# Optimization experiments

Measured on AMD Instinct MI355X. Metric: run time of the kernel, lower is better.

## Reference

```python
import jax, jax.numpy as jnp
import numpy as np

N_NODES = 50000
N_EDGES = 800000
IN_DIM = 128
HIDDEN = 32
NHEAD = 4
OUT_DIM = 64
NEG_SLOPE = 0.2


def setup_inputs() -> dict:
    key = jax.random.key(0)
    ks = jax.random.split(key, 8)
    x = jax.random.normal(ks[0], (N_NODES, IN_DIM), dtype=jnp.float32)
    edge_index = jax.random.randint(ks[1], (2, N_EDGES), 0, N_NODES, dtype=jnp.int64)
    # layer 1: fc (in_dim -> nhead*hidden), attn [nhead, 2*hidden]
    W1 = jax.random.normal(ks[2], (IN_DIM, NHEAD * HIDDEN), dtype=jnp.float32) * 0.1
    attn1 = jax.random.normal(ks[3], (NHEAD, 2 * HIDDEN), dtype=jnp.float32) * 0.1
    # layer 2: fc (nhead*hidden -> 1*out_dim), attn [1, 2*out_dim]
    W2 = jax.random.normal(ks[4], (NHEAD * HIDDEN, OUT_DIM), dtype=jnp.float32) * 0.1
    attn2 = jax.random.normal(ks[5], (1, 2 * OUT_DIM), dtype=jnp.float32) * 0.1
    # extra output head: Linear(out_dim, out_dim) with bias
    head_W = jax.random.normal(ks[6], (OUT_DIM, OUT_DIM), dtype=jnp.float32) * 0.1
    head_b = jax.random.normal(ks[7], (OUT_DIM,), dtype=jnp.float32) * 0.1
    return {"x": x, "edge_index": edge_index, "W1": W1, "attn1": attn1,
            "W2": W2, "attn2": attn2, "head_W": head_W, "head_b": head_b}


def _gat_layer(x, W, attn, row, col, num_nodes, heads):
    """One GATConv: linear proj, edge attention, segment softmax over dst (col), scatter-add."""
    f_out = W.shape[1] // heads
    h = (x @ W).reshape(num_nodes, heads, f_out)            # [N, H, F]
    a_l, a_r = attn[:, :f_out], attn[:, f_out:]              # split attn for src/dst parts
    e_src = jnp.einsum('nhf,hf->nh', h, a_l)                 # [N, H]
    e_dst = jnp.einsum('nhf,hf->nh', h, a_r)                 # [N, H]
    alpha = e_src[row] + e_dst[col]                          # [E, H] == cat(h[row],h[col])·attn
    alpha = jax.nn.leaky_relu(alpha, NEG_SLOPE)
    # segment softmax grouped by destination node (col); self-loops guarantee non-empty segs
    amax = jax.ops.segment_max(alpha, col, num_segments=num_nodes)
    ex = jnp.exp(alpha - amax[col])
    denom = jax.ops.segment_sum(ex, col, num_segments=num_nodes)
    a = ex / denom[col]                                      # [E, H]
    msg = h[row] * a[:, :, None]                             # [E, H, F]
    out = jax.ops.segment_sum(msg, col, num_segments=num_nodes)  # [N, H, F]
    return out.reshape(num_nodes, heads * f_out)


def reference(x, edge_index, W1, attn1, W2, attn2, head_W, head_b):
    n = x.shape[0]
    loops = jnp.arange(n, dtype=edge_index.dtype)
    row = jnp.concatenate([edge_index[0], loops])
    col = jnp.concatenate([edge_index[1], loops])
    h = _gat_layer(x, W1, attn1, row, col, n, NHEAD)         # [N, NHEAD*HIDDEN]
    h = jax.nn.relu(h)                                       # intermediate-layer activation
    h = _gat_layer(h, W2, attn2, row, col, n, 1)             # [N, OUT_DIM] (last: no act)
    out = h @ head_W + head_b                                # extra_output_fc head
    return out
```

## Files before the change

kernel.cpp:

```cpp
#include <hip/hip_runtime.h>
#include <math.h>

#define N_NODES 50000
#define E_RAW 800000
#define E_TOT 850000
#define NEG_SLOPE 0.2f
#define G1_BLOCKS ((N_NODES + 63) / 64)
#define NBUCK 391
#define EPB 2048
#define PBLK ((E_TOT + EPB - 1) / EPB)

typedef __attribute__((ext_vector_type(8))) short bf16x8;
typedef __attribute__((ext_vector_type(4))) float f32x4;

__device__ __forceinline__ float lrelu(float a) { return a > 0.f ? a : NEG_SLOPE * a; }

__device__ __forceinline__ unsigned f2bf(float f) {
    unsigned u = __float_as_uint(f);
    return (u + 0x7fff + ((u >> 16) & 1)) >> 16;
}
__device__ __forceinline__ unsigned pack2(float a, float b) {
    return f2bf(a) | (f2bf(b) << 16);
}
__device__ __forceinline__ float bflo(unsigned p) { return __uint_as_float(p << 16); }
__device__ __forceinline__ float bfhi(unsigned p) { return __uint_as_float(p & 0xffff0000u); }

__global__ void k_prep(const float* __restrict__ W1, unsigned* __restrict__ Btg) {
    int c = blockIdx.x;
    int tq = threadIdx.x;
    Btg[c * 64 + tq] = pack2(W1[(2 * tq) * 128 + c], W1[(2 * tq + 1) * 128 + c]);
}

__global__ void k_prep2(const float* __restrict__ W2, const float* __restrict__ attn2,
                        const float* __restrict__ headW,
                        unsigned* __restrict__ Wctg, float* __restrict__ av) {
    int b = blockIdx.x, t = threadIdx.x;
    if (b < 64) {
        if (t < 64) {
            int f = b, q = t;
            float s0 = 0.f, s1 = 0.f;
            for (int j = 0; j < 64; ++j) {
                float hw = headW[j * 64 + f];
                s0 = fmaf(W2[(2 * q) * 64 + j], hw, s0);
                s1 = fmaf(W2[(2 * q + 1) * 64 + j], hw, s1);
            }
            Wctg[f * 64 + q] = pack2(s0, s1);
        }
    } else {
        int k = t;
        float sl = 0.f, sr = 0.f;
        for (int j = 0; j < 64; ++j) {
            float w = W2[k * 64 + j];
            sl = fmaf(w, attn2[j], sl);
            sr = fmaf(w, attn2[64 + j], sr);
        }
        av[k] = sl; av[128 + k] = sr;
    }
}

__global__ void k_gemm1_p1(const float* __restrict__ A, const unsigned* __restrict__ Btg,
                           const float* __restrict__ aux, uint2* __restrict__ C,
                           float* __restrict__ es, float* __restrict__ ed,
                           const int* __restrict__ ei, int* __restrict__ hist2d) {
    __shared__ unsigned As[64 * 64];
    if (blockIdx.x >= G1_BLOCKS) {
        int blk = blockIdx.x - G1_BLOCKS;
        int* h = (int*)As;
        for (int i = threadIdx.x; i < NBUCK; i += 256) h[i] = 0;
        __syncthreads();
        int base = blk * EPB;
        for (int i = threadIdx.x; i < EPB; i += 256) {
            int e = base + i;
            if (e >= E_TOT) break;
            int col = (e < E_RAW) ? ei[E_RAW + e] : (e - E_RAW);
            atomicAdd(&h[col >> 7], 1);
        }
        __syncthreads();
        for (int i = threadIdx.x; i < NBUCK; i += 256) hist2d[i * PBLK + blk] = h[i];
        return;
    }
    int t = threadIdx.x;
    int m0 = blockIdx.x * 64;
    int rows = min(64, N_NODES - m0);
    const float4* A4 = (const float4*)(A + (size_t)m0 * 128);
    for (int i = t; i < rows * 32; i += 256) {
        int row = i >> 5, k4 = i & 31;
        float4 v = A4[i];
        int byte = (k4 * 8) ^ ((row & 7) << 4);
        unsigned* p = &As[row * 64 + (byte >> 2)];
        p[0] = pack2(v.x, v.y);
        p[1] = pack2(v.z, v.w);
    }
    __syncthreads();
    int lane = t & 63, wave = t >> 6;
    int r15 = lane & 15, g = lane >> 4;
    int arow = wave * 16 + r15;
    f32x4 acc[8];
#pragma unroll
    for (int i = 0; i < 8; ++i) acc[i] = (f32x4){0.f, 0.f, 0.f, 0.f};
    const char* Abase = (const char*)As + arow * 256;
    int swz = (arow & 7) << 4;
    const char* Bbase = (const char*)Btg;
#pragma unroll
    for (int s = 0; s < 4; ++s) {
        bf16x8 xf = *(const bf16x8*)(Abase + ((64 * s + 16 * g) ^ swz));
#pragma unroll
        for (int tt = 0; tt < 8; ++tt) {
            bf16x8 wf = *(const bf16x8*)(Bbase + ((16 * tt + r15) * 256 + 64 * s + 16 * g));
            acc[tt] = __builtin_amdgcn_mfma_f32_16x16x32_bf16(wf, xf, acc[tt], 0, 0, 0);
        }
    }
    int grow = m0 + arow;
    bool valid = (arow < rows);
    if (valid) {
        uint2* C2 = C + (size_t)grow * 32;
#pragma unroll
        for (int tt = 0; tt < 8; ++tt) {
            uint2 v; v.x = pack2(acc[tt][0], acc[tt][1]); v.y = pack2(acc[tt][2], acc[tt][3]);
            C2[4 * tt + g] = v;
        }
    }
    float ps0 = 0.f, ps1 = 0.f, ps2 = 0.f, ps3 = 0.f;
    float pd0 = 0.f, pd1 = 0.f, pd2 = 0.f, pd3 = 0.f;
#pragma unroll
    for (int tt = 0; tt < 8; ++tt) {
        int h = tt >> 1;
        int fin = 16 * (tt & 1) + 4 * g;
        float4 alv = *(const float4*)(aux + h * 64 + fin);
        float4 arv = *(const float4*)(aux + h * 64 + 32 + fin);
        float s4 = acc[tt][0] * alv.x + acc[tt][1] * alv.y + acc[tt][2] * alv.z + acc[tt][3] * alv.w;
        float d4 = acc[tt][0] * arv.x + acc[tt][1] * arv.y + acc[tt][2] * arv.z + acc[tt][3] * arv.w;
        if (h == 0) { ps0 += s4; pd0 += d4; }
        else if (h == 1) { ps1 += s4; pd1 += d4; }
        else if (h == 2) { ps2 += s4; pd2 += d4; }
        else { ps3 += s4; pd3 += d4; }
    }
#pragma unroll
    for (int mask = 16; mask <= 32; mask <<= 1) {
        ps0 += __shfl_xor(ps0, mask); ps1 += __shfl_xor(ps1, mask);
        ps2 += __shfl_xor(ps2, mask); ps3 += __shfl_xor(ps3, mask);
        pd0 += __shfl_xor(pd0, mask); pd1 += __shfl_xor(pd1, mask);
        pd2 += __shfl_xor(pd2, mask); pd3 += __shfl_xor(pd3, mask);
    }
    if (valid) {
        float psg = (g == 0) ? ps0 : (g == 1) ? ps1 : (g == 2) ? ps2 : ps3;
        float pdg = (g == 0) ? pd0 : (g == 1) ? pd1 : (g == 2) ? pd2 : pd3;
        es[grow * 4 + g] = psg;
        ed[grow * 4 + g] = pdg;
    }
}

__global__ void k_p2a(const int* __restrict__ hist2d, int* __restrict__ off2d,
                      int* __restrict__ bucktot) {
    __shared__ int sh[512];
    int b = blockIdx.x, t = threadIdx.x;
    int v = (t < PBLK) ? hist2d[b * PBLK + t] : 0;
    sh[t] = v;
    __syncthreads();
    for (int ofs = 1; ofs < 512; ofs <<= 1) {
        int u = (t >= ofs) ? sh[t - ofs] : 0;
        __syncthreads();
        sh[t] += u;
        __syncthreads();
    }
    if (t < PBLK) off2d[b * PBLK + t] = sh[t] - v;
    if (t == 511) bucktot[b] = sh[511];
}

__global__ void k_p3(const int* __restrict__ ei, const int* __restrict__ off2d,
                     const int* __restrict__ bucktot, unsigned* __restrict__ part) {
    __shared__ int sh[512];
    __shared__ int h[NBUCK];
    __shared__ int basebuf[NBUCK];
    int blk = blockIdx.x, t = threadIdx.x;
    int v = (t < NBUCK) ? bucktot[t] : 0;
    sh[t] = v;
    if (t < NBUCK) h[t] = 0;
    __syncthreads();
    for (int ofs = 1; ofs < 512; ofs <<= 1) {
        int u = (t >= ofs) ? sh[t - ofs] : 0;
        __syncthreads();
        sh[t] += u;
        __syncthreads();
    }
    if (t < NBUCK) basebuf[t] = (sh[t] - v) + off2d[t * PBLK + blk];
    __syncthreads();
    int base = blk * EPB;
    for (int i = t; i < EPB; i += 512) {
        int e = base + i;
        if (e >= E_TOT) break;
        int col, src;
        if (e < E_RAW) { col = ei[E_RAW + e]; src = ei[e]; }
        else { col = src = e - E_RAW; }
        int b = col >> 7;
        int lr = atomicAdd(&h[b], 1);
        part[basebuf[b] + lr] = (unsigned)src | ((unsigned)(col & 127) << 16);
    }
}

__global__ void k_p4(const unsigned* __restrict__ part, const int* __restrict__ bucktot,
                     int* __restrict__ off, unsigned short* __restrict__ srcs) {
    __shared__ int sh[512];
    __shared__ int h[128];
    __shared__ int colofs[128];
    __shared__ int s0sh, s1sh;
    int b = blockIdx.x, t = threadIdx.x;
    int v = (t < NBUCK) ? bucktot[t] : 0;
    sh[t] = v;
    if (t < 128) h[t] = 0;
    __syncthreads();
    for (int ofs = 1; ofs < 512; ofs <<= 1) {
        int u = (t >= ofs) ? sh[t - ofs] : 0;
        __syncthreads();
        sh[t] += u;
        __syncthreads();
    }
    if (t == 0) { s1sh = sh[b]; s0sh = sh[b] - bucktot[b]; }
    __syncthreads();
    int s0 = s0sh, s1 = s1sh;
    for (int i = s0 + t; i < s1; i += 512) atomicAdd(&h[part[i] >> 16], 1);
    __syncthreads();
    if (t == 0) {
        int acc = 0;
        for (int c = 0; c < 128; ++c) { colofs[c] = acc; acc += h[c]; }
    }
    __syncthreads();
    int colbase = b * 128, ncols = min(128, N_NODES - colbase);
    if (t < ncols) off[colbase + t] = s0 + colofs[t];
    if (b == NBUCK - 1 && t == 0) off[N_NODES] = s1;
    if (t < 128) h[t] = colofs[t];
    __syncthreads();
    for (int i = s0 + t; i < s1; i += 512) {
        unsigned u = part[i];
        int c = u >> 16;
        int slot = atomicAdd(&h[c], 1);
        srcs[s0 + slot] = (unsigned short)(u & 0xffffu);
    }
}

__global__ void k_gemmv(const unsigned* __restrict__ A, const unsigned* __restrict__ Wctg,
                        uint2* __restrict__ C) {
    __shared__ unsigned As[64 * 64];
    int t = threadIdx.x;
    int m0 = blockIdx.x * 64;
    int rows = min(64, N_NODES - m0);
    const uint4* A4 = (const uint4*)(A + (size_t)m0 * 64);
    for (int i = t; i < rows * 16; i += 256) {
        int row = i >> 4, q = i & 15;
        uint4 v = A4[i];
        int byte = (q * 16) ^ ((row & 7) << 4);
        unsigned* p = &As[row * 64 + (byte >> 2)];
        p[0] = v.x; p[1] = v.y; p[2] = v.z; p[3] = v.w;
    }
    __syncthreads();
    int lane = t & 63, wave = t >> 6;
    int r15 = lane & 15, g = lane >> 4;
    int arow = wave * 16 + r15;
    f32x4 acc[4];
#pragma unroll
    for (int i = 0; i < 4; ++i) acc[i] = (f32x4){0.f, 0.f, 0.f, 0.f};
    const char* Abase = (const char*)As + arow * 256;
    int swz = (arow & 7) << 4;
    const char* Bbase = (const char*)Wctg;
#pragma unroll
    for (int s = 0; s < 4; ++s) {
        bf16x8 xf = *(const bf16x8*)(Abase + ((64 * s + 16 * g) ^ swz));
#pragma unroll
        for (int tt = 0; tt < 4; ++tt) {
            bf16x8 wf = *(const bf16x8*)(Bbase + ((16 * tt + r15) * 256 + 64 * s + 16 * g));
            acc[tt] = __builtin_amdgcn_mfma_f32_16x16x32_bf16(wf, xf, acc[tt], 0, 0, 0);
        }
    }
    int grow = m0 + arow;
    if (arow < rows) {
        uint2* C2 = C + (size_t)grow * 16;
#pragma unroll
        for (int tt = 0; tt < 4; ++tt) {
            uint2 v; v.x = pack2(acc[tt][0], acc[tt][1]); v.y = pack2(acc[tt][2], acc[tt][3]);
            C2[4 * tt + g] = v;
        }
    }
}

__global__ void k_agg1(const unsigned* __restrict__ h1b, const float* __restrict__ es,
                       const float* __restrict__ ed, const int* __restrict__ off,
                       const unsigned short* __restrict__ srcs, const float* __restrict__ av,
                       unsigned* __restrict__ out1,
                       float* __restrict__ e2s, float* __restrict__ e2d) {
    int n = blockIdx.x * (blockDim.x >> 6) + (threadIdx.x >> 6);
    int lane = threadIdx.x & 63;
    if (n >= N_NODES) return;
    int myh = lane & 3;
    int jj = lane >> 2;
    float edh = ed[n * 4 + myh];
    int s = off[n], e = off[n + 1];
    int l16 = lane & 15;
    int esub = lane >> 4;
    int hcL = l16 >> 2;
    float acc[8];
#pragma unroll
    for (int i = 0; i < 8; ++i) acc[i] = 0.f;
    float psum = 0.f;
    for (int base = s; base < e; base += 16) {
        int cnt = e - base;
        int srcj = 0;
        float w = 0.f;
        if (jj < cnt) {
            srcj = srcs[base + jj];
            w = __expf(lrelu(es[srcj * 4 + myh] + edh));
        }
        psum += w;
        int src4[4];
        float wv4[4];
#pragma unroll
        for (int q = 0; q < 4; ++q) {
            int eidx = 4 * q + esub;
            src4[q] = __shfl(srcj, eidx * 4);
            wv4[q] = __shfl(w, eidx * 4 + hcL);
        }
        uint4 pv4[4];
#pragma unroll
        for (int q = 0; q < 4; ++q)
            pv4[q] = *((const uint4*)(h1b + (size_t)src4[q] * 64 + l16 * 4));
#pragma unroll
        for (int q = 0; q < 4; ++q) {
            float wv = wv4[q];
            acc[0] = fmaf(bflo(pv4[q].x), wv, acc[0]);
            acc[1] = fmaf(bfhi(pv4[q].x), wv, acc[1]);
            acc[2] = fmaf(bflo(pv4[q].y), wv, acc[2]);
            acc[3] = fmaf(bfhi(pv4[q].y), wv, acc[3]);
            acc[4] = fmaf(bflo(pv4[q].z), wv, acc[4]);
            acc[5] = fmaf(bfhi(pv4[q].z), wv, acc[5]);
            acc[6] = fmaf(bflo(pv4[q].w), wv, acc[6]);
            acc[7] = fmaf(bfhi(pv4[q].w), wv, acc[7]);
        }
    }
#pragma unroll
    for (int mask = 4; mask <= 32; mask <<= 1) psum += __shfl_xor(psum, mask);
    float inv = 1.f / __shfl(psum, hcL);
#pragma unroll
    for (int i = 0; i < 8; ++i) {
        acc[i] += __shfl_xor(acc[i], 16);
        acc[i] += __shfl_xor(acc[i], 32);
    }
    float o[8];
#pragma unroll
    for (int i = 0; i < 8; ++i) o[i] = fmaxf(acc[i] * inv, 0.f);
    if (esub == 0) {
        uint4 ov;
        ov.x = pack2(o[0], o[1]);
        ov.y = pack2(o[2], o[3]);
        ov.z = pack2(o[4], o[5]);
        ov.w = pack2(o[6], o[7]);
        *((uint4*)(out1 + (size_t)n * 64 + l16 * 4)) = ov;
    }
    float4 vl0 = *(const float4*)(av + 8 * l16);
    float4 vl1 = *(const float4*)(av + 8 * l16 + 4);
    float4 vr0 = *(const float4*)(av + 128 + 8 * l16);
    float4 vr1 = *(const float4*)(av + 128 + 8 * l16 + 4);
    float pl = o[0] * vl0.x + o[1] * vl0.y + o[2] * vl0.z + o[3] * vl0.w
             + o[4] * vl1.x + o[5] * vl1.y + o[6] * vl1.z + o[7] * vl1.w;
    float pr = o[0] * vr0.x + o[1] * vr0.y + o[2] * vr0.z + o[3] * vr0.w
             + o[4] * vr1.x + o[5] * vr1.y + o[6] * vr1.z + o[7] * vr1.w;
#pragma unroll
    for (int mask = 1; mask <= 8; mask <<= 1) {
        pl += __shfl_xor(pl, mask);
        pr += __shfl_xor(pr, mask);
    }
    if (lane == 0) { e2s[n] = pl; e2d[n] = pr; }
}

__global__ void k_agg2f(const unsigned* __restrict__ v2b, const float* __restrict__ es,
                        const float* __restrict__ ed, const int* __restrict__ off,
                        const unsigned short* __restrict__ srcs,
                        const float* __restrict__ headb, float* __restrict__ outv) {
    int n = blockIdx.x * 4 + (threadIdx.x >> 6);
    int lane = threadIdx.x & 63;
    float edv = ed[n];
    int s = off[n], e = off[n + 1];
    int l16 = lane & 15;
    int esub = lane >> 4;
    const uint2* gp = (const uint2*)v2b;
    float a0 = 0.f, a1 = 0.f, a2 = 0.f, a3 = 0.f, psum = 0.f;
    for (int base = s; base < e; base += 16) {
        int cnt = e - base;
        int srcj = 0;
        float w = 0.f;
        if (lane < 16 && lane < cnt) {
            srcj = srcs[base + lane];
            w = __expf(lrelu(es[srcj] + edv));
        }
        psum += w;
        int src4[4];
        float wv4[4];
#pragma unroll
        for (int q = 0; q < 4; ++q) {
            int eidx = 4 * q + esub;
            src4[q] = __shfl(srcj, eidx);
            wv4[q] = __shfl(w, eidx);
        }
        uint2 pv4[4];
#pragma unroll
        for (int q = 0; q < 4; ++q) pv4[q] = gp[(size_t)src4[q] * 16 + l16];
#pragma unroll
        for (int q = 0; q < 4; ++q) {
            a0 = fmaf(bflo(pv4[q].x), wv4[q], a0);
            a1 = fmaf(bfhi(pv4[q].x), wv4[q], a1);
            a2 = fmaf(bflo(pv4[q].y), wv4[q], a2);
            a3 = fmaf(bfhi(pv4[q].y), wv4[q], a3);
        }
    }
#pragma unroll
    for (int mask = 1; mask <= 8; mask <<= 1) psum += __shfl_xor(psum, mask);
    float inv = 1.f / __shfl(psum, 0);
    a0 += __shfl_xor(a0, 16); a0 += __shfl_xor(a0, 32);
    a1 += __shfl_xor(a1, 16); a1 += __shfl_xor(a1, 32);
    a2 += __shfl_xor(a2, 16); a2 += __shfl_xor(a2, 32);
    a3 += __shfl_xor(a3, 16); a3 += __shfl_xor(a3, 32);
    if (esub == 0) {
        float4 bv = ((const float4*)headb)[l16];
        float4 o;
        o.x = fmaf(a0, inv, bv.x);
        o.y = fmaf(a1, inv, bv.y);
        o.z = fmaf(a2, inv, bv.z);
        o.w = fmaf(a3, inv, bv.w);
        ((float4*)outv)[(size_t)n * 16 + l16] = o;
    }
}

extern "C" void kernel_launch(void* const* d_in, const int* in_sizes, int n_in,
                              void* d_out, int out_size, void* d_ws, size_t ws_size,
                              hipStream_t stream) {
    const float* x     = (const float*)d_in[0];
    const int*   ei    = (const int*)d_in[1];
    const float* W1    = (const float*)d_in[2];
    const float* attn1 = (const float*)d_in[3];
    const float* W2    = (const float*)d_in[4];
    const float* attn2 = (const float*)d_in[5];
    const float* headW = (const float*)d_in[6];
    const float* headb = (const float*)d_in[7];
    float* out = (float*)d_out;

    char* ws = (char*)d_ws;
    size_t o = 0;
    auto alloc = [&](size_t bytes) -> void* {
        o = (o + 255) & ~(size_t)255;
        void* p = ws + o;
        o += bytes;
        return p;
    };
    unsigned*       h1b    = (unsigned*)alloc((size_t)N_NODES * 128 * 2);
    unsigned*       out1b  = (unsigned*)alloc((size_t)N_NODES * 128 * 2);
    unsigned*       v2b    = (unsigned*)alloc((size_t)N_NODES * 64 * 2);
    float*          e1s    = (float*)alloc((size_t)N_NODES * 4 * 4);
    float*          e1d    = (float*)alloc((size_t)N_NODES * 4 * 4);
    float*          e2s    = (float*)alloc((size_t)N_NODES * 4);
    float*          e2d    = (float*)alloc((size_t)N_NODES * 4);
    int*            off    = (int*)alloc((size_t)(N_NODES + 1) * 4);
    unsigned short* srcs   = (unsigned short*)alloc((size_t)E_TOT * 2);
    unsigned*       Btg    = (unsigned*)alloc((size_t)128 * 64 * 4);
    unsigned*       Wctg   = (unsigned*)alloc((size_t)64 * 64 * 4);
    float*          av     = (float*)alloc((size_t)256 * 4);
    int*            hist2d = (int*)alloc((size_t)NBUCK * PBLK * 4);
    int*            off2d  = (int*)alloc((size_t)NBUCK * PBLK * 4);
    int*            bucktot = (int*)alloc((size_t)NBUCK * 4);
    unsigned*       part   = (unsigned*)alloc((size_t)E_TOT * 4);

    k_prep<<<128, 64, 0, stream>>>(W1, Btg);
    k_prep2<<<65, 128, 0, stream>>>(W2, attn2, headW, Wctg, av);

    k_gemm1_p1<<<G1_BLOCKS + PBLK, 256, 0, stream>>>(
        x, Btg, attn1, (uint2*)h1b, e1s, e1d, ei, hist2d);

    k_p2a<<<NBUCK, 512, 0, stream>>>(hist2d, off2d, bucktot);
    k_p3<<<PBLK, 512, 0, stream>>>(ei, off2d, bucktot, part);
    k_p4<<<NBUCK, 512, 0, stream>>>(part, bucktot, off, srcs);

    k_agg1<<<N_NODES / 4, 256, 0, stream>>>(h1b, e1s, e1d, off, srcs, av, out1b, e2s, e2d);

    k_gemmv<<<(N_NODES + 63) / 64, 256, 0, stream>>>(out1b, Wctg, (uint2*)v2b);

    k_agg2f<<<N_NODES / 4, 256, 0, stream>>>(v2b, e2s, e2d, off, srcs, headb, out);
}
```

Before: 209.4 us.

## Fuse CSR build passes into one cooperative kernel and merge prep kernels

Merges the three CSR-construction kernels (bucket scan, partition, per-column sort) into a single cooperative kernel that uses grid-wide syncs in place of kernel boundaries. The two weight-prep kernels become one launch. In both aggregation kernels the neighbour feature gathers are now issued before the attention-weight exp computation, so memory latency overlaps the math. This saves launch overhead at the cost of grid.sync barriers, and requires all PBLK blocks of 512 threads to be co-resident.

```diff
diff --git a/kernel.cpp b/kernel.cpp
--- a/kernel.cpp
+++ b/kernel.cpp
@@ -1,5 +1,8 @@
 #include <hip/hip_runtime.h>
+#include <hip/hip_cooperative_groups.h>
 #include <math.h>
+
+namespace cg = cooperative_groups;
 
 #define N_NODES 50000
 #define E_RAW 800000
@@ -25,19 +28,16 @@
 __device__ __forceinline__ float bflo(unsigned p) { return __uint_as_float(p << 16); }
 __device__ __forceinline__ float bfhi(unsigned p) { return __uint_as_float(p & 0xffff0000u); }
 
-__global__ void k_prep(const float* __restrict__ W1, unsigned* __restrict__ Btg) {
-    int c = blockIdx.x;
-    int tq = threadIdx.x;
-    Btg[c * 64 + tq] = pack2(W1[(2 * tq) * 128 + c], W1[(2 * tq + 1) * 128 + c]);
-}
-
-__global__ void k_prep2(const float* __restrict__ W2, const float* __restrict__ attn2,
-                        const float* __restrict__ headW,
-                        unsigned* __restrict__ Wctg, float* __restrict__ av) {
+__global__ void k_prep(const float* __restrict__ W1, const float* __restrict__ W2,
+                       const float* __restrict__ attn2, const float* __restrict__ headW,
+                       unsigned* __restrict__ Btg, unsigned* __restrict__ Wctg,
+                       float* __restrict__ av) {
     int b = blockIdx.x, t = threadIdx.x;
-    if (b < 64) {
+    if (b < 128) {
+        if (t < 64) Btg[b * 64 + t] = pack2(W1[(2 * t) * 128 + b], W1[(2 * t + 1) * 128 + b]);
+    } else if (b < 192) {
         if (t < 64) {
-            int f = b, q = t;
+            int f = b - 128, q = t;
             float s0 = 0.f, s1 = 0.f;
             for (int j = 0; j < 64; ++j) {
                 float hw = headW[j * 64 + f];
@@ -150,91 +150,88 @@
     }
 }
 
-__global__ void k_p2a(const int* __restrict__ hist2d, int* __restrict__ off2d,
-                      int* __restrict__ bucktot) {
+__global__ void k_csr(const int* __restrict__ ei, const int* __restrict__ hist2d,
+                      int* __restrict__ off2d, int* __restrict__ bucktot,
+                      unsigned* __restrict__ part, int* __restrict__ off,
+                      unsigned short* __restrict__ srcs) {
+    cg::grid_group grid = cg::this_grid();
     __shared__ int sh[512];
-    int b = blockIdx.x, t = threadIdx.x;
-    int v = (t < PBLK) ? hist2d[b * PBLK + t] : 0;
-    sh[t] = v;
-    __syncthreads();
-    for (int ofs = 1; ofs < 512; ofs <<= 1) {
-        int u = (t >= ofs) ? sh[t - ofs] : 0;
-        __syncthreads();
-        sh[t] += u;
-        __syncthreads();
-    }
-    if (t < PBLK) off2d[b * PBLK + t] = sh[t] - v;
-    if (t == 511) bucktot[b] = sh[511];
-}
-
-__global__ void k_p3(const int* __restrict__ ei, const int* __restrict__ off2d,
-                     const int* __restrict__ bucktot, unsigned* __restrict__ part) {
-    __shared__ int sh[512];
-    __shared__ int h[NBUCK];
-    __shared__ int basebuf[NBUCK];
-    int blk = blockIdx.x, t = threadIdx.x;
-    int v = (t < NBUCK) ? bucktot[t] : 0;
-    sh[t] = v;
-    if (t < NBUCK) h[t] = 0;
-    __syncthreads();
-    for (int ofs = 1; ofs < 512; ofs <<= 1) {
-        int u = (t >= ofs) ? sh[t - ofs] : 0;
-        __syncthreads();
-        sh[t] += u;
-        __syncthreads();
-    }
-    if (t < NBUCK) basebuf[t] = (sh[t] - v) + off2d[t * PBLK + blk];
-    __syncthreads();
-    int base = blk * EPB;
-    for (int i = t; i < EPB; i += 512) {
-        int e = base + i;
-        if (e >= E_TOT) break;
-        int col, src;
-        if (e < E_RAW) { col = ei[E_RAW + e]; src = ei[e]; }
-        else { col = src = e - E_RAW; }
-        int b = col >> 7;
-        int lr = atomicAdd(&h[b], 1);
-        part[basebuf[b] + lr] = (unsigned)src | ((unsigned)(col & 127) << 16);
-    }
-}
-
-__global__ void k_p4(const unsigned* __restrict__ part, const int* __restrict__ bucktot,
-                     int* __restrict__ off, unsigned short* __restrict__ srcs) {
-    __shared__ int sh[512];
-    __shared__ int h[128];
-    __shared__ int colofs[128];
+    __shared__ int hh[NBUCK];
+    __shared__ int bb[NBUCK];
     __shared__ int s0sh, s1sh;
     int b = blockIdx.x, t = threadIdx.x;
-    int v = (t < NBUCK) ? bucktot[t] : 0;
-    sh[t] = v;
-    if (t < 128) h[t] = 0;
-    __syncthreads();
-    for (int ofs = 1; ofs < 512; ofs <<= 1) {
-        int u = (t >= ofs) ? sh[t - ofs] : 0;
-        __syncthreads();
-        sh[t] += u;
-        __syncthreads();
-    }
-    if (t == 0) { s1sh = sh[b]; s0sh = sh[b] - bucktot[b]; }
-    __syncthreads();
-    int s0 = s0sh, s1 = s1sh;
-    for (int i = s0 + t; i < s1; i += 512) atomicAdd(&h[part[i] >> 16], 1);
-    __syncthreads();
-    if (t == 0) {
-        int acc = 0;
-        for (int c = 0; c < 128; ++c) { colofs[c] = acc; acc += h[c]; }
-    }
-    __syncthreads();
-    int colbase = b * 128, ncols = min(128, N_NODES - colbase);
-    if (t < ncols) off[colbase + t] = s0 + colofs[t];
-    if (b == NBUCK - 1 && t == 0) off[N_NODES] = s1;
-    if (t < 128) h[t] = colofs[t];
-    __syncthreads();
-    for (int i = s0 + t; i < s1; i += 512) {
-        unsigned u = part[i];
-        int c = u >> 16;
-        int slot = atomicAdd(&h[c], 1);
-        srcs[s0 + slot] = (unsigned short)(u & 0xffffu);
+    if (b < NBUCK) {
+        int v = (t < PBLK) ? hist2d[b * PBLK + t] : 0;
+        sh[t] = v;
+        __syncthreads();
+        for (int ofs = 1; ofs < 512; ofs <<= 1) {
+            int u = (t >= ofs) ? sh[t - ofs] : 0;
+            __syncthreads();
+            sh[t] += u;
+            __syncthreads();
+        }
+        if (t < PBLK) off2d[b * PBLK + t] = sh[t] - v;
+        if (t == 511) bucktot[b] = sh[511];
+    }
+    grid.sync();
+    if (b < PBLK) {
+        int v = (t < NBUCK) ? bucktot[t] : 0;
+        sh[t] = v;
+        if (t < NBUCK) hh[t] = 0;
+        __syncthreads();
+        for (int ofs = 1; ofs < 512; ofs <<= 1) {
+            int u = (t >= ofs) ? sh[t - ofs] : 0;
+            __syncthreads();
+            sh[t] += u;
+            __syncthreads();
+        }
+        if (t < NBUCK) bb[t] = (sh[t] - v) + off2d[t * PBLK + b];
+        __syncthreads();
+        int base = b * EPB;
+        for (int i = t; i < EPB; i += 512) {
+            int e = base + i;
+            if (e >= E_TOT) break;
+            int col, src;
+            if (e < E_RAW) { col = ei[E_RAW + e]; src = ei[e]; }
+            else { col = src = e - E_RAW; }
+            int bk = col >> 7;
+            int lr = atomicAdd(&hh[bk], 1);
+            part[bb[bk] + lr] = (unsigned)src | ((unsigned)(col & 127) << 16);
+        }
+    }
+    grid.sync();
+    if (b < NBUCK) {
+        int v = (t < NBUCK) ? bucktot[t] : 0;
+        sh[t] = v;
+        if (t < 128) hh[t] = 0;
+        __syncthreads();
+        for (int ofs = 1; ofs < 512; ofs <<= 1) {
+            int u = (t >= ofs) ? sh[t - ofs] : 0;
+            __syncthreads();
+            sh[t] += u;
+            __syncthreads();
+        }
+        if (t == 0) { s1sh = sh[b]; s0sh = sh[b] - bucktot[b]; }
+        __syncthreads();
+        int s0 = s0sh, s1 = s1sh;
+        for (int i = s0 + t; i < s1; i += 512) atomicAdd(&hh[part[i] >> 16], 1);
+        __syncthreads();
+        if (t == 0) {
+            int acc = 0;
+            for (int c = 0; c < 128; ++c) { bb[c] = acc; acc += hh[c]; }
+        }
+        __syncthreads();
+        int colbase = b * 128, ncols = min(128, N_NODES - colbase);
+        if (t < ncols) off[colbase + t] = s0 + bb[t];
+        if (b == NBUCK - 1 && t == 0) off[N_NODES] = s1;
+        if (t < 128) hh[t] = bb[t];
+        __syncthreads();
+        for (int i = s0 + t; i < s1; i += 512) {
+            unsigned u = part[i];
+            int c = u >> 16;
+            int slot = atomicAdd(&hh[c], 1);
+            srcs[s0 + slot] = (unsigned short)(u & 0xffffu);
+        }
     }
 }
 
@@ -304,24 +301,20 @@
     for (int base = s; base < e; base += 16) {
         int cnt = e - base;
         int srcj = 0;
-        float w = 0.f;
-        if (jj < cnt) {
-            srcj = srcs[base + jj];
-            w = __expf(lrelu(es[srcj * 4 + myh] + edh));
-        }
-        psum += w;
+        if (jj < cnt) srcj = srcs[base + jj];
         int src4[4];
-        float wv4[4];
-#pragma unroll
-        for (int q = 0; q < 4; ++q) {
-            int eidx = 4 * q + esub;
-            src4[q] = __shfl(srcj, eidx * 4);
-            wv4[q] = __shfl(w, eidx * 4 + hcL);
-        }
+#pragma unroll
+        for (int q = 0; q < 4; ++q) src4[q] = __shfl(srcj, (4 * q + esub) * 4);
         uint4 pv4[4];
 #pragma unroll
         for (int q = 0; q < 4; ++q)
             pv4[q] = *((const uint4*)(h1b + (size_t)src4[q] * 64 + l16 * 4));
+        float w = 0.f;
+        if (jj < cnt) w = __expf(lrelu(es[srcj * 4 + myh] + edh));
+        psum += w;
+        float wv4[4];
+#pragma unroll
+        for (int q = 0; q < 4; ++q) wv4[q] = __shfl(w, (4 * q + esub) * 4 + hcL);
 #pragma unroll
         for (int q = 0; q < 4; ++q) {
             float wv = wv4[q];
@@ -385,23 +378,19 @@
     for (int base = s; base < e; base += 16) {
         int cnt = e - base;
         int srcj = 0;
+        if (lane < 16 && lane < cnt) srcj = srcs[base + lane];
+        int src4[4];
+#pragma unroll
+        for (int q = 0; q < 4; ++q) src4[q] = __shfl(srcj, 4 * q + esub);
+        uint2 pv4[4];
+#pragma unroll
+        for (int q = 0; q < 4; ++q) pv4[q] = gp[(size_t)src4[q] * 16 + l16];
         float w = 0.f;
-        if (lane < 16 && lane < cnt) {
-            srcj = srcs[base + lane];
-            w = __expf(lrelu(es[srcj] + edv));
-        }
+        if (lane < 16 && lane < cnt) w = __expf(lrelu(es[srcj] + edv));
         psum += w;
-        int src4[4];
         float wv4[4];
 #pragma unroll
-        for (int q = 0; q < 4; ++q) {
-            int eidx = 4 * q + esub;
-            src4[q] = __shfl(srcj, eidx);
-            wv4[q] = __shfl(w, eidx);
-        }
-        uint2 pv4[4];
-#pragma unroll
-        for (int q = 0; q < 4; ++q) pv4[q] = gp[(size_t)src4[q] * 16 + l16];
+        for (int q = 0; q < 4; ++q) wv4[q] = __shfl(w, 4 * q + esub);
 #pragma unroll
         for (int q = 0; q < 4; ++q) {
             a0 = fmaf(bflo(pv4[q].x), wv4[q], a0);
@@ -466,15 +455,17 @@
     int*            bucktot = (int*)alloc((size_t)NBUCK * 4);
     unsigned*       part   = (unsigned*)alloc((size_t)E_TOT * 4);
 
-    k_prep<<<128, 64, 0, stream>>>(W1, Btg);
-    k_prep2<<<65, 128, 0, stream>>>(W2, attn2, headW, Wctg, av);
+    k_prep<<<193, 128, 0, stream>>>(W1, W2, attn2, headW, Btg, Wctg, av);
 
     k_gemm1_p1<<<G1_BLOCKS + PBLK, 256, 0, stream>>>(
         x, Btg, attn1, (uint2*)h1b, e1s, e1d, ei, hist2d);
 
-    k_p2a<<<NBUCK, 512, 0, stream>>>(hist2d, off2d, bucktot);
-    k_p3<<<PBLK, 512, 0, stream>>>(ei, off2d, bucktot, part);
-    k_p4<<<NBUCK, 512, 0, stream>>>(part, bucktot, off, srcs);
+    {
+        void* csr_args[] = {(void*)&ei, (void*)&hist2d, (void*)&off2d, (void*)&bucktot,
+                            (void*)&part, (void*)&off, (void*)&srcs};
+        (void)hipLaunchCooperativeKernel((void*)k_csr, dim3(PBLK), dim3(512),
+                                         csr_args, 0, stream);
+    }
 
     k_agg1<<<N_NODES / 4, 256, 0, stream>>>(h1b, e1s, e1d, off, srcs, av, out1b, e2s, e2d);
 
```

Result: slower. 332.8 us (+59.0%).
